# Kernel optimization log

Measured on AMD Instinct MI355X. Metric: run time of the kernel, lower is better.

Reference implementation:

```python
import jax, jax.numpy as jnp
import numpy as np

B, C, H, W, K = 2, 36, 512, 512, 9
GROUPS, GSIZE = 3, 12  # channel groups 0:12, 12:24, 24:36


def _grid_sample_bilinear(feat, gx, gy):
    """Bilinear grid_sample, align_corners=True. feat [B,C,H,W]; gx,gy [B,H,W] in [-1,1]."""
    Bn, Cn, Hn, Wn = feat.shape
    px = (gx + 1.0) * 0.5 * (Wn - 1)
    py = (gy + 1.0) * 0.5 * (Hn - 1)
    x0 = jnp.floor(px)
    y0 = jnp.floor(py)
    wx = (px - x0)[:, None, :, :]
    wy = (py - y0)[:, None, :, :]
    x0i = jnp.clip(x0.astype(jnp.int32), 0, Wn - 1)
    x1i = jnp.clip(x0i + 1, 0, Wn - 1)
    y0i = jnp.clip(y0.astype(jnp.int32), 0, Hn - 1)
    y1i = jnpip = jnp.clip(y0.astype(jnp.int32) + 1, 0, Hn - 1)
    flat = feat.reshape(Bn, Cn, Hn * Wn)
    gather = jax.vmap(lambda f, yi, xi: f[:, yi * Wn + xi])  # -> [B,C,H,W]
    v00 = gather(flat, y0i, x0i)
    v01 = gather(flat, y0i, x1i)
    v10 = gather(flat, y1i, x0i)
    v11 = gather(flat, y1i, x1i)
    return (v00 * (1 - wx) * (1 - wy) + v01 * wx * (1 - wy)
            + v10 * (1 - wx) * wy + v11 * wx * wy)


def setup_inputs() -> dict:
    key = jax.random.key(0)
    k1, k2, k3 = jax.random.split(key, 3)
    features = jax.random.normal(k1, (B, C, H, W), jnp.float32)
    offset_x = jax.random.normal(k2, (B, K, H, W), jnp.float32) * 16.0
    offset_y = jax.random.normal(k3, (B, K, H, W), jnp.float32) * 16.0
    left_x = jnp.broadcast_to(jnp.arange(W, dtype=jnp.float32)[None, None, None, :], (B, 1, H, W))
    left_y = jnp.broadcast_to(jnp.arange(H, dtype=jnp.float32)[None, None, :, None], (B, 1, H, W))
    return {"features": features, "offset_x": offset_x, "offset_y": offset_y,
            "left_x": jnp.array(left_x), "left_y": jnp.array(left_y)}


def reference(features, offset_x, offset_y, left_x, left_y):
    Hn, Wn = features.shape[2], features.shape[3]
    # clamp candidate coords to image, then normalize to [-1,1]
    rx = jnp.clip(left_x + offset_x, 0.0, Wn - 1)
    ry = jnp.clip(left_y + offset_y, 0.0, Hn - 1)
    gx = (rx - (Wn - 1) / 2.0) / ((Wn - 1) / 2.0)  # [B,K,H,W]
    gy = (ry - (Hn - 1) / 2.0) / ((Hn - 1) / 2.0)

    def per_candidate(g):
        gxk, gyk = g  # each [B,H,W]
        a = _grid_sample_bilinear(features, gxk, gyk)  # [B,36,H,W]
        a2 = jnp.roll(a, 12, axis=1)
        a3 = jnp.roll(a, 24, axis=1)

        def grp_mean(d):  # [B,36,H,W] -> [B,3,H,W] mean over 12-channel groups
            return d.reshape(d.shape[0], GROUPS, GSIZE, d.shape[2], d.shape[3]).mean(axis=2)

        s = jnp.concatenate([grp_mean(-jnp.abs(features - a)),
                             grp_mean(-jnp.abs(features - a2)),
                             grp_mean(-jnp.abs(features - a3))], axis=1)  # [B,9,H,W]
        return jnp.max(s, axis=1)  # top-1 of sort == max  -> [B,H,W]

    strengths = jax.lax.map(per_candidate,
                            (jnp.moveaxis(gx, 1, 0), jnp.moveaxis(gy, 1, 0)))  # [K,B,H,W]
    strengths = jnp.moveaxis(strengths, 0, 1)  # [B,K,H,W]

    wgt = jax.nn.softmax(strengths * 1000.0, axis=1)
    ox = jnp.sum(offset_x * wgt, axis=1, keepdims=True)
    oy = jnp.sum(offset_y * wgt, axis=1, keepdims=True)
    oy = jnp.clip(oy + left_y, 0.0, Hn - 1) - left_y
    ox = jnp.clip(ox + left_x, 0.0, Wn - 1) - left_x
    return ox, oy
```

## Files before the change

kernel.cpp:

```cpp
#include <hip/hip_runtime.h>
#include <math.h>

#define B_ 2
#define C_ 36
#define H_ 512
#define W_ 512
#define K_ 9
#define HW_ (H_ * W_)
#define ROWF4 (W_ * C_ / 4)

__global__ __launch_bounds__(256) void transpose_kernel(const float* __restrict__ in,
                                                        float* __restrict__ out) {
  __shared__ float tile[64][37];
  int blk = blockIdx.x;
  int wt = blk & 7;
  int h = (blk >> 3) & (H_ - 1);
  int b = blk >> 12;
  int w0 = wt << 6;
  int tid = threadIdx.x;
  const float* src = in + ((size_t)b * C_) * HW_ + (size_t)h * W_ + w0;
#pragma unroll
  for (int it = 0; it < 9; ++it) {
    int idx = it * 256 + tid;
    int c = idx >> 6;
    int wl = idx & 63;
    tile[wl][c] = src[(size_t)c * HW_ + wl];
  }
  __syncthreads();
  float* dst = out + (((size_t)b * H_ + h) * W_ + w0) * C_;
#pragma unroll
  for (int it = 0; it < 9; ++it) {
    int idx = it * 256 + tid;
    int wl = idx / 36;
    int c = idx - wl * 36;
    dst[idx] = tile[wl][c];
  }
}

__global__ __launch_bounds__(64, 2) void eval_kernel_cw(const float* __restrict__ feat,
                                                        const float* __restrict__ offx,
                                                        const float* __restrict__ offy,
                                                        float* __restrict__ out) {
  __shared__ __align__(16) float scratch[32 * 36];
  __shared__ __align__(16) float4 w_lds[64];
  __shared__ int a_lds[64];

  int tid = threadIdx.x;
  int blk = blockIdx.x;
  int region = blk & 7;
  int slot = blk >> 3;
  int b = region >> 2;
  int qd = region & 3;
  int qy = (qd >> 1) << 8;
  int qx = (qd & 1) << 8;
  int tr = slot >> 5;
  int tc = slot & 31;
  if (tr & 1) tc = 31 - tc;
  int h = qy + tr * 8 + (tid >> 3);
  int w = qx + tc * 8 + (tid & 7);
  int ph = h * W_ + w;
  int p = b * HW_ + ph;

  const float4* feat4 = reinterpret_cast<const float4*>(feat);

  const float* oxb = offx + (size_t)b * K_ * HW_ + ph;
  const float* oyb = offy + (size_t)b * K_ * HW_ + ph;
  float oxv[K_], oyv[K_];
#pragma unroll
  for (int k = 0; k < K_; ++k) {
    oxv[k] = oxb[k * HW_];
    oyv[k] = oyb[k * HW_];
  }

  float F[C_];
  {
    const float4* myF = feat4 + (size_t)p * 9;
#pragma unroll
    for (int i = 0; i < 9; ++i) {
      float4 v = myF[i];
      F[4 * i + 0] = v.x; F[4 * i + 1] = v.y; F[4 * i + 2] = v.z; F[4 * i + 3] = v.w;
    }
  }

  int g = tid / 9;
  int q = tid - 9 * g;

  float lx = (float)w;
  float ly = (float)h;

  float M = -INFINITY, den = 0.f, axs = 0.f, ays = 0.f;

#pragma unroll 1
  for (int k = 0; k < K_; ++k) {
    float ox = oxv[k];
    float oy = oyv[k];
    float rx = fminf(fmaxf(lx + ox, 0.0f), 511.0f);
    float ry = fminf(fmaxf(ly + oy, 0.0f), 511.0f);
    float gx = (rx - 255.5f) / 255.5f;
    float gy = (ry - 255.5f) / 255.5f;
    float px = (gx + 1.0f) * 0.5f * 511.0f;
    float py = (gy + 1.0f) * 0.5f * 511.0f;
    int x0 = (int)floorf(px); x0 = (x0 > 510) ? 510 : x0;
    int y0 = (int)floorf(py); y0 = (y0 > 510) ? 510 : y0;
    float wx = px - (float)x0;
    float wy = py - (float)y0;
    w_lds[tid] = make_float4((1.0f - wx) * (1.0f - wy), wx * (1.0f - wy),
                             (1.0f - wx) * wy, wx * wy);
    a_lds[tid] = ((b * H_ + y0) * W_ + x0) * 9;
    __syncthreads();

    float4 L[5][4];
#pragma unroll
    for (int r = 0; r < 5; ++r) {
      int tt = 7 * r + g;
      int t = (tt > 31) ? 31 : tt;
      const float4* r0 = feat4 + a_lds[t];
      L[r][0] = r0[q];
      L[r][1] = r0[9 + q];
      L[r][2] = r0[ROWF4 + q];
      L[r][3] = r0[ROWF4 + 9 + q];
    }
#pragma unroll
    for (int r = 0; r < 5; ++r) {
      int tt = 7 * r + g;
      int t = (tt > 31) ? 31 : tt;
      float4 W4 = w_lds[t];
      float4 v00 = L[r][0], v01 = L[r][1], v10 = L[r][2], v11 = L[r][3];
      float4 a4;
      a4.x = W4.x * v00.x + W4.y * v01.x + W4.z * v10.x + W4.w * v11.x;
      a4.y = W4.x * v00.y + W4.y * v01.y + W4.z * v10.y + W4.w * v11.y;
      a4.z = W4.x * v00.z + W4.y * v01.z + W4.z * v10.z + W4.w * v11.z;
      a4.w = W4.x * v00.w + W4.y * v01.w + W4.z * v10.w + W4.w * v11.w;
      if (tt < 32 && tid < 63) {
        *reinterpret_cast<float4*>(&scratch[t * 36 + 4 * q]) = a4;
      }
    }
#pragma unroll
    for (int r = 0; r < 5; ++r) {
      int tt = 32 + 7 * r + g;
      int t = (tt > 63) ? 63 : tt;
      const float4* r0 = feat4 + a_lds[t];
      L[r][0] = r0[q];
      L[r][1] = r0[9 + q];
      L[r][2] = r0[ROWF4 + q];
      L[r][3] = r0[ROWF4 + 9 + q];
    }
    if (tid < 32) {
      float D[9] = {0.f, 0.f, 0.f, 0.f, 0.f, 0.f, 0.f, 0.f, 0.f};
      const float4* sc = reinterpret_cast<const float4*>(&scratch[tid * 36]);
#pragma unroll
      for (int q2 = 0; q2 < 9; ++q2) {
        float4 a4 = sc[q2];
        float av[4] = {a4.x, a4.y, a4.z, a4.w};
        int ga = q2 / 3;
        int f0 = 4 * (q2 % 3);
#pragma unroll
        for (int j = 0; j < 4; ++j) {
          D[ga]     += fabsf(F[f0 + j]      - av[j]);
          D[3 + ga] += fabsf(F[12 + f0 + j] - av[j]);
          D[6 + ga] += fabsf(F[24 + f0 + j] - av[j]);
        }
      }
      float mn = D[0];
#pragma unroll
      for (int j = 1; j < 9; ++j) mn = fminf(mn, D[j]);
      float xk = -(mn / 12.0f) * 1000.0f;
      float nm = fmaxf(M, xk);
      float scl = expf(M - nm);
      float ek = expf(xk - nm);
      den = den * scl + ek;
      axs = axs * scl + ox * ek;
      ays = ays * scl + oy * ek;
      M = nm;
    }
#pragma unroll
    for (int r = 0; r < 5; ++r) {
      int tt = 32 + 7 * r + g;
      int t = (tt > 63) ? 63 : tt;
      float4 W4 = w_lds[t];
      float4 v00 = L[r][0], v01 = L[r][1], v10 = L[r][2], v11 = L[r][3];
      float4 a4;
      a4.x = W4.x * v00.x + W4.y * v01.x + W4.z * v10.x + W4.w * v11.x;
      a4.y = W4.x * v00.y + W4.y * v01.y + W4.z * v10.y + W4.w * v11.y;
      a4.z = W4.x * v00.z + W4.y * v01.z + W4.z * v10.z + W4.w * v11.z;
      a4.w = W4.x * v00.w + W4.y * v01.w + W4.z * v10.w + W4.w * v11.w;
      if (tt < 64 && tid < 63) {
        *reinterpret_cast<float4*>(&scratch[(t - 32) * 36 + 4 * q]) = a4;
      }
    }
    if (tid >= 32) {
      float D[9] = {0.f, 0.f, 0.f, 0.f, 0.f, 0.f, 0.f, 0.f, 0.f};
      const float4* sc = reinterpret_cast<const float4*>(&scratch[(tid - 32) * 36]);
#pragma unroll
      for (int q2 = 0; q2 < 9; ++q2) {
        float4 a4 = sc[q2];
        float av[4] = {a4.x, a4.y, a4.z, a4.w};
        int ga = q2 / 3;
        int f0 = 4 * (q2 % 3);
#pragma unroll
        for (int j = 0; j < 4; ++j) {
          D[ga]     += fabsf(F[f0 + j]      - av[j]);
          D[3 + ga] += fabsf(F[12 + f0 + j] - av[j]);
          D[6 + ga] += fabsf(F[24 + f0 + j] - av[j]);
        }
      }
      float mn = D[0];
#pragma unroll
      for (int j = 1; j < 9; ++j) mn = fminf(mn, D[j]);
      float xk = -(mn / 12.0f) * 1000.0f;
      float nm = fmaxf(M, xk);
      float scl = expf(M - nm);
      float ek = expf(xk - nm);
      den = den * scl + ek;
      axs = axs * scl + ox * ek;
      ays = ays * scl + oy * ek;
      M = nm;
    }
  }

  float resx = axs / den;
  float resy = ays / den;
  out[p] = fminf(fmaxf(resx + lx, 0.0f), 511.0f) - lx;
  out[B_ * HW_ + p] = fminf(fmaxf(resy + ly, 0.0f), 511.0f) - ly;
}

__global__ __launch_bounds__(256) void eval_kernel_n(const float* __restrict__ feat,
                                                     const float* __restrict__ offx,
                                                     const float* __restrict__ offy,
                                                     float* __restrict__ out) {
  int p = blockIdx.x * 256 + threadIdx.x;
  int ph = p & (HW_ - 1);
  int b = p >> 18;
  float F[C_];
  const float* fb = feat + (size_t)b * C_ * HW_ + ph;
#pragma unroll
  for (int c = 0; c < C_; ++c) F[c] = fb[(size_t)c * HW_];
  float lx = (float)(ph & (W_ - 1));
  float ly = (float)((ph >> 9) & (H_ - 1));
  const float* oxb = offx + (size_t)b * K_ * HW_ + ph;
  const float* oyb = offy + (size_t)b * K_ * HW_ + ph;
  float M = -INFINITY, den = 0.f, ax = 0.f, ay = 0.f;
#pragma unroll 1
  for (int k = 0; k < K_; ++k) {
    float ox = oxb[k * HW_];
    float oy = oyb[k * HW_];
    float rx = fminf(fmaxf(lx + ox, 0.0f), 511.0f);
    float ry = fminf(fmaxf(ly + oy, 0.0f), 511.0f);
    float gx = (rx - 255.5f) / 255.5f;
    float gy = (ry - 255.5f) / 255.5f;
    float px = (gx + 1.0f) * 0.5f * 511.0f;
    float py = (gy + 1.0f) * 0.5f * 511.0f;
    int x0 = (int)floorf(px); x0 = (x0 > 510) ? 510 : x0;
    int y0 = (int)floorf(py); y0 = (y0 > 510) ? 510 : y0;
    float wx = px - (float)x0;
    float wy = py - (float)y0;
    float w00 = (1.0f - wx) * (1.0f - wy);
    float w01 = wx * (1.0f - wy);
    float w10 = (1.0f - wx) * wy;
    float w11 = wx * wy;
    float D[9] = {0.f, 0.f, 0.f, 0.f, 0.f, 0.f, 0.f, 0.f, 0.f};
    const float* pl = feat + (size_t)b * C_ * HW_ + (size_t)y0 * W_ + x0;
#pragma unroll
    for (int c = 0; c < C_; ++c) {
      const float* q0 = pl + (size_t)c * HW_;
      float v00 = q0[0], v01 = q0[1];
      float v10 = q0[W_], v11 = q0[W_ + 1];
      float a = v00 * w00 + v01 * w01 + v10 * w10 + v11 * w11;
      int i = c % 12;
      int ga = c / 12;
      D[ga]     += fabsf(F[i]      - a);
      D[3 + ga] += fabsf(F[12 + i] - a);
      D[6 + ga] += fabsf(F[24 + i] - a);
    }
    float mn = D[0];
#pragma unroll
    for (int j = 1; j < 9; ++j) mn = fminf(mn, D[j]);
    float xk = -(mn / 12.0f) * 1000.0f;
    float nm = fmaxf(M, xk);
    float sc = expf(M - nm);
    float ek = expf(xk - nm);
    den = den * sc + ek;
    ax = ax * sc + ox * ek;
    ay = ay * sc + oy * ek;
    M = nm;
  }
  float resx = ax / den;
  float resy = ay / den;
  out[p] = fminf(fmaxf(resx + lx, 0.0f), 511.0f) - lx;
  out[B_ * HW_ + p] = fminf(fmaxf(resy + ly, 0.0f), 511.0f) - ly;
}

extern "C" void kernel_launch(void* const* d_in, const int* in_sizes, int n_in,
                              void* d_out, int out_size, void* d_ws, size_t ws_size,
                              hipStream_t stream) {
  const float* features = (const float*)d_in[0];
  const float* offset_x = (const float*)d_in[1];
  const float* offset_y = (const float*)d_in[2];
  float* out = (float*)d_out;

  const int npix = B_ * HW_;
  const size_t need = (size_t)npix * C_ * sizeof(float);

  if (ws_size >= need) {
    float* featT = (float*)d_ws;
    transpose_kernel<<<B_ * H_ * (W_ / 64), 256, 0, stream>>>(features, featT);
    eval_kernel_cw<<<npix / 64, 64, 0, stream>>>(featT, offset_x, offset_y, out);
  } else {
    eval_kernel_n<<<npix / 256, 256, 0, stream>>>(features, offset_x, offset_y, out);
  }
}
```

Baseline: 311.5 us.

## Replace cooperative LDS-staged gather with per-thread bilinear gather over 256-pixel rows

The cooperative wave-level scheme, where 64 threads jointly fetched the neighbours' 36-channel corners through LDS scratch with barriers, is replaced. Each thread now gathers its own four corner rows as float4 loads and accumulates the group distances directly in registers. Blocks now cover 256 consecutive pixels of one row instead of 8x8 tiles, and launch bounds become 256 threads with 4 blocks. This removes the LDS traffic, the syncs and the redundant clamped work. The cost is uncoalesced per-thread strided gathers (144 bytes per corner per thread), higher register pressure, and worse 2D locality for random offsets.

```diff
diff --git a/kernel.cpp b/kernel.cpp
--- a/kernel.cpp
+++ b/kernel.cpp
@@ -37,27 +37,18 @@
   }
 }
 
-__global__ __launch_bounds__(64, 2) void eval_kernel_cw(const float* __restrict__ feat,
-                                                        const float* __restrict__ offx,
-                                                        const float* __restrict__ offy,
-                                                        float* __restrict__ out) {
-  __shared__ __align__(16) float scratch[32 * 36];
-  __shared__ __align__(16) float4 w_lds[64];
-  __shared__ int a_lds[64];
-
+__global__ __launch_bounds__(256, 4) void eval_kernel_tp(const float* __restrict__ feat,
+                                                         const float* __restrict__ offx,
+                                                         const float* __restrict__ offy,
+                                                         float* __restrict__ out) {
   int tid = threadIdx.x;
   int blk = blockIdx.x;
   int region = blk & 7;
   int slot = blk >> 3;
   int b = region >> 2;
   int qd = region & 3;
-  int qy = (qd >> 1) << 8;
-  int qx = (qd & 1) << 8;
-  int tr = slot >> 5;
-  int tc = slot & 31;
-  if (tr & 1) tc = 31 - tc;
-  int h = qy + tr * 8 + (tid >> 3);
-  int w = qx + tc * 8 + (tid & 7);
+  int h = ((qd >> 1) << 8) + slot;
+  int w = ((qd & 1) << 8) + tid;
   int ph = h * W_ + w;
   int p = b * HW_ + ph;
 
@@ -81,9 +72,6 @@
       F[4 * i + 0] = v.x; F[4 * i + 1] = v.y; F[4 * i + 2] = v.z; F[4 * i + 3] = v.w;
     }
   }
-
-  int g = tid / 9;
-  int q = tid - 9 * g;
 
   float lx = (float)w;
   float ly = (float)h;
@@ -104,118 +92,51 @@
     int y0 = (int)floorf(py); y0 = (y0 > 510) ? 510 : y0;
     float wx = px - (float)x0;
     float wy = py - (float)y0;
-    w_lds[tid] = make_float4((1.0f - wx) * (1.0f - wy), wx * (1.0f - wy),
-                             (1.0f - wx) * wy, wx * wy);
-    a_lds[tid] = ((b * H_ + y0) * W_ + x0) * 9;
-    __syncthreads();
-
-    float4 L[5][4];
-#pragma unroll
-    for (int r = 0; r < 5; ++r) {
-      int tt = 7 * r + g;
-      int t = (tt > 31) ? 31 : tt;
-      const float4* r0 = feat4 + a_lds[t];
-      L[r][0] = r0[q];
-      L[r][1] = r0[9 + q];
-      L[r][2] = r0[ROWF4 + q];
-      L[r][3] = r0[ROWF4 + 9 + q];
+    float w00 = (1.0f - wx) * (1.0f - wy);
+    float w01 = wx * (1.0f - wy);
+    float w10 = (1.0f - wx) * wy;
+    float w11 = wx * wy;
+
+    const float4* r0 = feat4 + (size_t)(((b * H_ + y0) * W_ + x0) * 9);
+
+    float D[9] = {0.f, 0.f, 0.f, 0.f, 0.f, 0.f, 0.f, 0.f, 0.f};
+#pragma unroll
+    for (int q = 0; q < 9; ++q) {
+      float4 v00 = r0[q];
+      float4 v01 = r0[9 + q];
+      float4 v10 = r0[ROWF4 + q];
+      float4 v11 = r0[ROWF4 + 9 + q];
+      float a0 = w00 * v00.x + w01 * v01.x + w10 * v10.x + w11 * v11.x;
+      float a1 = w00 * v00.y + w01 * v01.y + w10 * v10.y + w11 * v11.y;
+      float a2 = w00 * v00.z + w01 * v01.z + w10 * v10.z + w11 * v11.z;
+      float a3 = w00 * v00.w + w01 * v01.w + w10 * v10.w + w11 * v11.w;
+      int ga = q / 3;
+      int f0 = 4 * (q % 3);
+      D[ga]     += fabsf(F[f0 + 0]      - a0);
+      D[3 + ga] += fabsf(F[12 + f0 + 0] - a0);
+      D[6 + ga] += fabsf(F[24 + f0 + 0] - a0);
+      D[ga]     += fabsf(F[f0 + 1]      - a1);
+      D[3 + ga] += fabsf(F[12 + f0 + 1] - a1);
+      D[6 + ga] += fabsf(F[24 + f0 + 1] - a1);
+      D[ga]     += fabsf(F[f0 + 2]      - a2);
+      D[3 + ga] += fabsf(F[12 + f0 + 2] - a2);
+      D[6 + ga] += fabsf(F[24 + f0 + 2] - a2);
+      D[ga]     += fabsf(F[f0 + 3]      - a3);
+      D[3 + ga] += fabsf(F[12 + f0 + 3] - a3);
+      D[6 + ga] += fabsf(F[24 + f0 + 3] - a3);
     }
-#pragma unroll
-    for (int r = 0; r < 5; ++r) {
-      int tt = 7 * r + g;
-      int t = (tt > 31) ? 31 : tt;
-      float4 W4 = w_lds[t];
-      float4 v00 = L[r][0], v01 = L[r][1], v10 = L[r][2], v11 = L[r][3];
-      float4 a4;
-      a4.x = W4.x * v00.x + W4.y * v01.x + W4.z * v10.x + W4.w * v11.x;
-      a4.y = W4.x * v00.y + W4.y * v01.y + W4.z * v10.y + W4.w * v11.y;
-      a4.z = W4.x * v00.z + W4.y * v01.z + W4.z * v10.z + W4.w * v11.z;
-      a4.w = W4.x * v00.w + W4.y * v01.w + W4.z * v10.w + W4.w * v11.w;
-      if (tt < 32 && tid < 63) {
-        *reinterpret_cast<float4*>(&scratch[t * 36 + 4 * q]) = a4;
-      }
-    }
-#pragma unroll
-    for (int r = 0; r < 5; ++r) {
-      int tt = 32 + 7 * r + g;
-      int t = (tt > 63) ? 63 : tt;
-      const float4* r0 = feat4 + a_lds[t];
-      L[r][0] = r0[q];
-      L[r][1] = r0[9 + q];
-      L[r][2] = r0[ROWF4 + q];
-      L[r][3] = r0[ROWF4 + 9 + q];
-    }
-    if (tid < 32) {
-      float D[9] = {0.f, 0.f, 0.f, 0.f, 0.f, 0.f, 0.f, 0.f, 0.f};
-      const float4* sc = reinterpret_cast<const float4*>(&scratch[tid * 36]);
-#pragma unroll
-      for (int q2 = 0; q2 < 9; ++q2) {
-        float4 a4 = sc[q2];
-        float av[4] = {a4.x, a4.y, a4.z, a4.w};
-        int ga = q2 / 3;
-        int f0 = 4 * (q2 % 3);
-#pragma unroll
-        for (int j = 0; j < 4; ++j) {
-          D[ga]     += fabsf(F[f0 + j]      - av[j]);
-          D[3 + ga] += fabsf(F[12 + f0 + j] - av[j]);
-          D[6 + ga] += fabsf(F[24 + f0 + j] - av[j]);
-        }
-      }
-      float mn = D[0];
-#pragma unroll
-      for (int j = 1; j < 9; ++j) mn = fminf(mn, D[j]);
-      float xk = -(mn / 12.0f) * 1000.0f;
-      float nm = fmaxf(M, xk);
-      float scl = expf(M - nm);
-      float ek = expf(xk - nm);
-      den = den * scl + ek;
-      axs = axs * scl + ox * ek;
-      ays = ays * scl + oy * ek;
-      M = nm;
-    }
-#pragma unroll
-    for (int r = 0; r < 5; ++r) {
-      int tt = 32 + 7 * r + g;
-      int t = (tt > 63) ? 63 : tt;
-      float4 W4 = w_lds[t];
-      float4 v00 = L[r][0], v01 = L[r][1], v10 = L[r][2], v11 = L[r][3];
-      float4 a4;
-      a4.x = W4.x * v00.x + W4.y * v01.x + W4.z * v10.x + W4.w * v11.x;
-      a4.y = W4.x * v00.y + W4.y * v01.y + W4.z * v10.y + W4.w * v11.y;
-      a4.z = W4.x * v00.z + W4.y * v01.z + W4.z * v10.z + W4.w * v11.z;
-      a4.w = W4.x * v00.w + W4.y * v01.w + W4.z * v10.w + W4.w * v11.w;
-      if (tt < 64 && tid < 63) {
-        *reinterpret_cast<float4*>(&scratch[(t - 32) * 36 + 4 * q]) = a4;
-      }
-    }
-    if (tid >= 32) {
-      float D[9] = {0.f, 0.f, 0.f, 0.f, 0.f, 0.f, 0.f, 0.f, 0.f};
-      const float4* sc = reinterpret_cast<const float4*>(&scratch[(tid - 32) * 36]);
-#pragma unroll
-      for (int q2 = 0; q2 < 9; ++q2) {
-        float4 a4 = sc[q2];
-        float av[4] = {a4.x, a4.y, a4.z, a4.w};
-        int ga = q2 / 3;
-        int f0 = 4 * (q2 % 3);
-#pragma unroll
-        for (int j = 0; j < 4; ++j) {
-          D[ga]     += fabsf(F[f0 + j]      - av[j]);
-          D[3 + ga] += fabsf(F[12 + f0 + j] - av[j]);
-          D[6 + ga] += fabsf(F[24 + f0 + j] - av[j]);
-        }
-      }
-      float mn = D[0];
-#pragma unroll
-      for (int j = 1; j < 9; ++j) mn = fminf(mn, D[j]);
-      float xk = -(mn / 12.0f) * 1000.0f;
-      float nm = fmaxf(M, xk);
-      float scl = expf(M - nm);
-      float ek = expf(xk - nm);
-      den = den * scl + ek;
-      axs = axs * scl + ox * ek;
-      ays = ays * scl + oy * ek;
-      M = nm;
-    }
+
+    float mn = D[0];
+#pragma unroll
+    for (int j = 1; j < 9; ++j) mn = fminf(mn, D[j]);
+    float xk = -(mn / 12.0f) * 1000.0f;
+    float nm = fmaxf(M, xk);
+    float scl = expf(M - nm);
+    float ek = expf(xk - nm);
+    den = den * scl + ek;
+    axs = axs * scl + ox * ek;
+    ays = ays * scl + oy * ek;
+    M = nm;
   }
 
   float resx = axs / den;
@@ -304,7 +225,7 @@
   if (ws_size >= need) {
     float* featT = (float*)d_ws;
     transpose_kernel<<<B_ * H_ * (W_ / 64), 256, 0, stream>>>(features, featT);
-    eval_kernel_cw<<<npix / 64, 64, 0, stream>>>(featT, offset_x, offset_y, out);
+    eval_kernel_tp<<<npix / 256, 256, 0, stream>>>(featT, offset_x, offset_y, out);
   } else {
     eval_kernel_n<<<npix / 256, 256, 0, stream>>>(features, offset_x, offset_y, out);
   }
```

After: 919.1 us. 2.95x slower.

## Split candidates across three waves per block and widen transpose tiles

Applied to the files above, without the earlier changes.

The eval kernel now runs 192 threads per block. Each of three wavefronts handles three of the nine candidates for the same 64 pixels, and the partial online-softmax states are merged through LDS at the end. The per-candidate block barrier is removed, since each wave now uses its own scratch. This trades more redundant per-pixel feature loads and larger LDS use for more parallelism and latency hiding. The transpose kernel is also reworked to move 256-pixel strips with float4 stores.

```diff
diff --git a/kernel.cpp b/kernel.cpp
--- a/kernel.cpp
+++ b/kernel.cpp
@@ -9,43 +9,44 @@
 #define HW_ (H_ * W_)
 #define ROWF4 (W_ * C_ / 4)
 
-__global__ __launch_bounds__(256) void transpose_kernel(const float* __restrict__ in,
-                                                        float* __restrict__ out) {
-  __shared__ float tile[64][37];
+__global__ __launch_bounds__(256) void transpose_kernel2(const float* __restrict__ in,
+                                                         float* __restrict__ out) {
+  __shared__ float tile[256][37];
   int blk = blockIdx.x;
-  int wt = blk & 7;
-  int h = (blk >> 3) & (H_ - 1);
-  int b = blk >> 12;
-  int w0 = wt << 6;
+  int strip = blk & 1;
+  int h = (blk >> 1) & (H_ - 1);
+  int b = blk >> 10;
+  int w0 = strip << 8;
   int tid = threadIdx.x;
-  const float* src = in + ((size_t)b * C_) * HW_ + (size_t)h * W_ + w0;
+  const float* src = in + (size_t)b * C_ * HW_ + (size_t)h * W_ + w0;
+#pragma unroll
+  for (int c = 0; c < C_; ++c) {
+    tile[tid][c] = src[(size_t)c * HW_ + tid];
+  }
+  __syncthreads();
+  float4* dst = reinterpret_cast<float4*>(out + (((size_t)b * H_ + h) * W_ + w0) * C_);
 #pragma unroll
   for (int it = 0; it < 9; ++it) {
     int idx = it * 256 + tid;
-    int c = idx >> 6;
-    int wl = idx & 63;
-    tile[wl][c] = src[(size_t)c * HW_ + wl];
-  }
-  __syncthreads();
-  float* dst = out + (((size_t)b * H_ + h) * W_ + w0) * C_;
-#pragma unroll
-  for (int it = 0; it < 9; ++it) {
-    int idx = it * 256 + tid;
-    int wl = idx / 36;
-    int c = idx - wl * 36;
-    dst[idx] = tile[wl][c];
+    int px = idx / 9;
+    int qq = idx - 9 * px;
+    dst[idx] = make_float4(tile[px][4 * qq + 0], tile[px][4 * qq + 1],
+                           tile[px][4 * qq + 2], tile[px][4 * qq + 3]);
   }
 }
 
-__global__ __launch_bounds__(64, 2) void eval_kernel_cw(const float* __restrict__ feat,
-                                                        const float* __restrict__ offx,
-                                                        const float* __restrict__ offy,
-                                                        float* __restrict__ out) {
-  __shared__ __align__(16) float scratch[32 * 36];
-  __shared__ __align__(16) float4 w_lds[64];
-  __shared__ int a_lds[64];
+__global__ __launch_bounds__(192, 4) void eval_kernel_ks(const float* __restrict__ feat,
+                                                         const float* __restrict__ offx,
+                                                         const float* __restrict__ offy,
+                                                         float* __restrict__ out) {
+  __shared__ __align__(16) float scratch[3][32 * 36];
+  __shared__ __align__(16) float4 w_lds[3][64];
+  __shared__ int a_lds[3][64];
 
   int tid = threadIdx.x;
+  int wv = tid >> 6;
+  int ln = tid & 63;
+
   int blk = blockIdx.x;
   int region = blk & 7;
   int slot = blk >> 3;
@@ -56,8 +57,8 @@
   int tr = slot >> 5;
   int tc = slot & 31;
   if (tr & 1) tc = 31 - tc;
-  int h = qy + tr * 8 + (tid >> 3);
-  int w = qx + tc * 8 + (tid & 7);
+  int h = qy + tr * 8 + (ln >> 3);
+  int w = qx + tc * 8 + (ln & 7);
   int ph = h * W_ + w;
   int p = b * HW_ + ph;
 
@@ -65,11 +66,11 @@
 
   const float* oxb = offx + (size_t)b * K_ * HW_ + ph;
   const float* oyb = offy + (size_t)b * K_ * HW_ + ph;
-  float oxv[K_], oyv[K_];
-#pragma unroll
-  for (int k = 0; k < K_; ++k) {
-    oxv[k] = oxb[k * HW_];
-    oyv[k] = oyb[k * HW_];
+  float oxv[3], oyv[3];
+#pragma unroll
+  for (int j = 0; j < 3; ++j) {
+    oxv[j] = oxb[(3 * wv + j) * HW_];
+    oyv[j] = oyb[(3 * wv + j) * HW_];
   }
 
   float F[C_];
@@ -82,18 +83,20 @@
     }
   }
 
-  int g = tid / 9;
-  int q = tid - 9 * g;
+  int g = ln / 9;
+  int q = ln - 9 * g;
 
   float lx = (float)w;
   float ly = (float)h;
 
   float M = -INFINITY, den = 0.f, axs = 0.f, ays = 0.f;
 
+  float* myScr = scratch[wv];
+
 #pragma unroll 1
-  for (int k = 0; k < K_; ++k) {
-    float ox = oxv[k];
-    float oy = oyv[k];
+  for (int j = 0; j < 3; ++j) {
+    float ox = oxv[j];
+    float oy = oyv[j];
     float rx = fminf(fmaxf(lx + ox, 0.0f), 511.0f);
     float ry = fminf(fmaxf(ly + oy, 0.0f), 511.0f);
     float gx = (rx - 255.5f) / 255.5f;
@@ -104,17 +107,16 @@
     int y0 = (int)floorf(py); y0 = (y0 > 510) ? 510 : y0;
     float wx = px - (float)x0;
     float wy = py - (float)y0;
-    w_lds[tid] = make_float4((1.0f - wx) * (1.0f - wy), wx * (1.0f - wy),
-                             (1.0f - wx) * wy, wx * wy);
-    a_lds[tid] = ((b * H_ + y0) * W_ + x0) * 9;
-    __syncthreads();
+    w_lds[wv][ln] = make_float4((1.0f - wx) * (1.0f - wy), wx * (1.0f - wy),
+                                (1.0f - wx) * wy, wx * wy);
+    a_lds[wv][ln] = ((b * H_ + y0) * W_ + x0) * 9;
 
     float4 L[5][4];
 #pragma unroll
     for (int r = 0; r < 5; ++r) {
       int tt = 7 * r + g;
       int t = (tt > 31) ? 31 : tt;
-      const float4* r0 = feat4 + a_lds[t];
+      const float4* r0 = feat4 + a_lds[wv][t];
       L[r][0] = r0[q];
       L[r][1] = r0[9 + q];
       L[r][2] = r0[ROWF4 + q];
@@ -124,30 +126,30 @@
     for (int r = 0; r < 5; ++r) {
       int tt = 7 * r + g;
       int t = (tt > 31) ? 31 : tt;
-      float4 W4 = w_lds[t];
+      float4 W4 = w_lds[wv][t];
       float4 v00 = L[r][0], v01 = L[r][1], v10 = L[r][2], v11 = L[r][3];
       float4 a4;
       a4.x = W4.x * v00.x + W4.y * v01.x + W4.z * v10.x + W4.w * v11.x;
       a4.y = W4.x * v00.y + W4.y * v01.y + W4.z * v10.y + W4.w * v11.y;
       a4.z = W4.x * v00.z + W4.y * v01.z + W4.z * v10.z + W4.w * v11.z;
       a4.w = W4.x * v00.w + W4.y * v01.w + W4.z * v10.w + W4.w * v11.w;
-      if (tt < 32 && tid < 63) {
-        *reinterpret_cast<float4*>(&scratch[t * 36 + 4 * q]) = a4;
+      if (tt < 32 && ln < 63) {
+        *reinterpret_cast<float4*>(&myScr[t * 36 + 4 * q]) = a4;
       }
     }
 #pragma unroll
     for (int r = 0; r < 5; ++r) {
       int tt = 32 + 7 * r + g;
       int t = (tt > 63) ? 63 : tt;
-      const float4* r0 = feat4 + a_lds[t];
+      const float4* r0 = feat4 + a_lds[wv][t];
       L[r][0] = r0[q];
       L[r][1] = r0[9 + q];
       L[r][2] = r0[ROWF4 + q];
       L[r][3] = r0[ROWF4 + 9 + q];
     }
-    if (tid < 32) {
+    if (ln < 32) {
       float D[9] = {0.f, 0.f, 0.f, 0.f, 0.f, 0.f, 0.f, 0.f, 0.f};
-      const float4* sc = reinterpret_cast<const float4*>(&scratch[tid * 36]);
+      const float4* sc = reinterpret_cast<const float4*>(&myScr[ln * 36]);
 #pragma unroll
       for (int q2 = 0; q2 < 9; ++q2) {
         float4 a4 = sc[q2];
@@ -155,15 +157,15 @@
         int ga = q2 / 3;
         int f0 = 4 * (q2 % 3);
 #pragma unroll
-        for (int j = 0; j < 4; ++j) {
-          D[ga]     += fabsf(F[f0 + j]      - av[j]);
-          D[3 + ga] += fabsf(F[12 + f0 + j] - av[j]);
-          D[6 + ga] += fabsf(F[24 + f0 + j] - av[j]);
+        for (int jj = 0; jj < 4; ++jj) {
+          D[ga]     += fabsf(F[f0 + jj]      - av[jj]);
+          D[3 + ga] += fabsf(F[12 + f0 + jj] - av[jj]);
+          D[6 + ga] += fabsf(F[24 + f0 + jj] - av[jj]);
         }
       }
       float mn = D[0];
 #pragma unroll
-      for (int j = 1; j < 9; ++j) mn = fminf(mn, D[j]);
+      for (int jj = 1; jj < 9; ++jj) mn = fminf(mn, D[jj]);
       float xk = -(mn / 12.0f) * 1000.0f;
       float nm = fmaxf(M, xk);
       float scl = expf(M - nm);
@@ -177,20 +179,20 @@
     for (int r = 0; r < 5; ++r) {
       int tt = 32 + 7 * r + g;
       int t = (tt > 63) ? 63 : tt;
-      float4 W4 = w_lds[t];
+      float4 W4 = w_lds[wv][t];
       float4 v00 = L[r][0], v01 = L[r][1], v10 = L[r][2], v11 = L[r][3];
       float4 a4;
       a4.x = W4.x * v00.x + W4.y * v01.x + W4.z * v10.x + W4.w * v11.x;
       a4.y = W4.x * v00.y + W4.y * v01.y + W4.z * v10.y + W4.w * v11.y;
       a4.z = W4.x * v00.z + W4.y * v01.z + W4.z * v10.z + W4.w * v11.z;
       a4.w = W4.x * v00.w + W4.y * v01.w + W4.z * v10.w + W4.w * v11.w;
-      if (tt < 64 && tid < 63) {
-        *reinterpret_cast<float4*>(&scratch[(t - 32) * 36 + 4 * q]) = a4;
+      if (tt < 64 && ln < 63) {
+        *reinterpret_cast<float4*>(&myScr[(t - 32) * 36 + 4 * q]) = a4;
       }
     }
-    if (tid >= 32) {
+    if (ln >= 32) {
       float D[9] = {0.f, 0.f, 0.f, 0.f, 0.f, 0.f, 0.f, 0.f, 0.f};
-      const float4* sc = reinterpret_cast<const float4*>(&scratch[(tid - 32) * 36]);
+      const float4* sc = reinterpret_cast<const float4*>(&myScr[(ln - 32) * 36]);
 #pragma unroll
       for (int q2 = 0; q2 < 9; ++q2) {
         float4 a4 = sc[q2];
@@ -198,15 +200,15 @@
         int ga = q2 / 3;
         int f0 = 4 * (q2 % 3);
 #pragma unroll
-        for (int j = 0; j < 4; ++j) {
-          D[ga]     += fabsf(F[f0 + j]      - av[j]);
-          D[3 + ga] += fabsf(F[12 + f0 + j] - av[j]);
-          D[6 + ga] += fabsf(F[24 + f0 + j] - av[j]);
+        for (int jj = 0; jj < 4; ++jj) {
+          D[ga]     += fabsf(F[f0 + jj]      - av[jj]);
+          D[3 + ga] += fabsf(F[12 + f0 + jj] - av[jj]);
+          D[6 + ga] += fabsf(F[24 + f0 + jj] - av[jj]);
         }
       }
       float mn = D[0];
 #pragma unroll
-      for (int j = 1; j < 9; ++j) mn = fminf(mn, D[j]);
+      for (int jj = 1; jj < 9; ++jj) mn = fminf(mn, D[jj]);
       float xk = -(mn / 12.0f) * 1000.0f;
       float nm = fmaxf(M, xk);
       float scl = expf(M - nm);
@@ -218,10 +220,24 @@
     }
   }
 
-  float resx = axs / den;
-  float resy = ays / den;
-  out[p] = fminf(fmaxf(resx + lx, 0.0f), 511.0f) - lx;
-  out[B_ * HW_ + p] = fminf(fmaxf(resy + ly, 0.0f), 511.0f) - ly;
+  *reinterpret_cast<float4*>(&myScr[ln * 4]) = make_float4(M, den, axs, ays);
+  __syncthreads();
+  if (wv == 0) {
+    float4 s0 = *reinterpret_cast<const float4*>(&scratch[0][ln * 4]);
+    float4 s1 = *reinterpret_cast<const float4*>(&scratch[1][ln * 4]);
+    float4 s2 = *reinterpret_cast<const float4*>(&scratch[2][ln * 4]);
+    float nm = fmaxf(s0.x, fmaxf(s1.x, s2.x));
+    float e0 = expf(s0.x - nm);
+    float e1 = expf(s1.x - nm);
+    float e2 = expf(s2.x - nm);
+    float dent = s0.y * e0 + s1.y * e1 + s2.y * e2;
+    float ax = s0.z * e0 + s1.z * e1 + s2.z * e2;
+    float ay = s0.w * e0 + s1.w * e1 + s2.w * e2;
+    float resx = ax / dent;
+    float resy = ay / dent;
+    out[p] = fminf(fmaxf(resx + lx, 0.0f), 511.0f) - lx;
+    out[B_ * HW_ + p] = fminf(fmaxf(resy + ly, 0.0f), 511.0f) - ly;
+  }
 }
 
 __global__ __launch_bounds__(256) void eval_kernel_n(const float* __restrict__ feat,
@@ -303,8 +319,8 @@
 
   if (ws_size >= need) {
     float* featT = (float*)d_ws;
-    transpose_kernel<<<B_ * H_ * (W_ / 64), 256, 0, stream>>>(features, featT);
-    eval_kernel_cw<<<npix / 64, 64, 0, stream>>>(featT, offset_x, offset_y, out);
+    transpose_kernel2<<<B_ * H_ * 2, 256, 0, stream>>>(features, featT);
+    eval_kernel_ks<<<npix / 64, 192, 0, stream>>>(featT, offset_x, offset_y, out);
   } else {
     eval_kernel_n<<<npix / 256, 256, 0, stream>>>(features, offset_x, offset_y, out);
   }
```

New measurement: 546.3 us. 75.4% more time.
